# Optimization experiments

Measured on AMD Instinct MI355X. Metric: run time of the kernel, lower is better.

## Reference

```python
import jax, jax.numpy as jnp
import numpy as np

B, N, DIM = 4, 2048, 256
H, HD, M = 8, 32, 4
SPARSE_TOPK = 32


def setup_inputs() -> dict:
    key = jax.random.key(0)
    ks = jax.random.split(key, 6)
    x = jax.random.normal(ks[0], (B, N, DIM), dtype=jnp.float32)
    w_qkv = jax.random.normal(ks[1], (DIM, 3 * H * HD), dtype=jnp.float32) * 0.02
    b_qkv = jnp.zeros((3 * H * HD,), dtype=jnp.float32)
    w_proj = jax.random.normal(ks[2], (H * HD, DIM), dtype=jnp.float32) * 0.02
    b_proj = jnp.zeros((DIM,), dtype=jnp.float32)
    scale = jnp.ones((1, H, 1, 1), dtype=jnp.float32)  # trainable scale, init scale_value=1.0
    mem_k = jax.random.normal(ks[3], (H, M, HD), dtype=jnp.float32)
    mem_v = jax.random.normal(ks[4], (H, M, HD), dtype=jnp.float32)
    return {"x": x, "w_qkv": w_qkv, "b_qkv": b_qkv, "w_proj": w_proj,
            "b_proj": b_proj, "scale": scale, "mem_k": mem_k, "mem_v": mem_v}


def reference(x, w_qkv, b_qkv, w_proj, b_proj, scale, mem_k, mem_v):
    b, n, dim = x.shape
    h, m, hd = mem_k.shape
    qkv = (x @ w_qkv + b_qkv).reshape(b, n, 3, h, hd).transpose(2, 0, 3, 1, 4)
    q, k, v = qkv[0], qkv[1], qkv[2]
    # concat memory vectors along key-length axis -> [B,H,N+M,hd]
    k = jnp.concatenate([k, jnp.broadcast_to(mem_k, (b, h, m, hd))], axis=2)
    v = jnp.concatenate([v, jnp.broadcast_to(mem_v, (b, h, m, hd))], axis=2)
    s = n + m
    # scores with trainable per-head scale: [B,H,N,S]
    scores = jnp.einsum('bhnd,bhsd->bhns', q, k) * (hd ** -0.5) * scale
    neg = -jnp.finfo(scores.dtype).max
    # improve_locality: mask rectangular diagonal (eye(N, S))
    diag = jnp.arange(n)[:, None] == jnp.arange(s)[None, :]
    scores = jnp.where(diag, neg, scores)
    # sparse topk: keep only values >= k-th largest per row
    top = jax.lax.top_k(scores, SPARSE_TOPK)[0]
    vk = top[..., -1:]
    scores = jnp.where(scores < vk, neg, scores)
    attn = jax.nn.softmax(scores, axis=-1)
    out = jnp.einsum('bhns,bhsd->bhnd', attn, v)
    out = out.transpose(0, 2, 1, 3).reshape(b, n, h * hd)
    return out @ w_proj + b_proj
```

## Files before the change

kernel.cpp:

```cpp
#include <hip/hip_runtime.h>
#include <float.h>
#include <stdint.h>

#define Bb   4
#define Nn   2048
#define DIMc 256
#define Hh   8
#define HDd  32
#define Mm   4
#define STOT 2052
#define ROWS 8
#define SROW 2112
#define NVROW 2052

typedef float f32x2 __attribute__((ext_vector_type(2)));

__device__ __forceinline__ unsigned int f2key(float s) {
    unsigned int b = __float_as_uint(s);
    return (b & 0x80000000u) ? ~b : (b | 0x80000000u);
}
__device__ __forceinline__ float key2f(unsigned int u) {
    unsigned int b = (u & 0x80000000u) ? (u ^ 0x80000000u) : ~u;
    return __uint_as_float(b);
}

__global__ __launch_bounds__(256) void sgemm_qkv(
    const float* __restrict__ A, const float* __restrict__ Bm,
    const float* __restrict__ bias, float* __restrict__ Qb,
    float* __restrict__ kTb, float* __restrict__ Vx,
    const float* __restrict__ memv)
{
    __shared__ __align__(16) float As[16][68];
    __shared__ __align__(16) float Bs[16][64];
    __shared__ __align__(16) float Ts[64][65];
    const int tid = threadIdx.x;
    const int tx = tid & 15, ty = tid >> 4;
    const int m0 = blockIdx.y * 64, n0 = blockIdx.x * 64;
    const int arow = tid >> 2, acol = (tid & 3) * 4;
    const int brow = tid >> 4, bcol = (tid & 15) * 4;
    float acc[4][4] = {};
    for (int kb = 0; kb < DIMc; kb += 16) {
        const float4 av = *(const float4*)&A[(size_t)(m0 + arow) * DIMc + kb + acol];
        const float4 bv = *(const float4*)&Bm[(size_t)(kb + brow) * 768 + n0 + bcol];
        __syncthreads();
        As[acol + 0][arow] = av.x;
        As[acol + 1][arow] = av.y;
        As[acol + 2][arow] = av.z;
        As[acol + 3][arow] = av.w;
        *(float4*)&Bs[brow][bcol] = bv;
        __syncthreads();
#pragma unroll
        for (int k = 0; k < 16; ++k) {
            const float4 a  = *(const float4*)&As[k][ty * 4];
            const float4 bq = *(const float4*)&Bs[k][tx * 4];
            const float aa[4] = {a.x, a.y, a.z, a.w};
            const float bb[4] = {bq.x, bq.y, bq.z, bq.w};
#pragma unroll
            for (int i = 0; i < 4; ++i)
#pragma unroll
                for (int j = 0; j < 4; ++j)
                    acc[i][j] = fmaf(aa[i], bb[j], acc[i][j]);
        }
    }
    const float4 bv = *(const float4*)&bias[n0 + tx * 4];
    const float bb[4] = {bv.x, bv.y, bv.z, bv.w};
    const int path = n0 >> 8;
    if (path == 1) {
#pragma unroll
        for (int i = 0; i < 4; ++i)
#pragma unroll
            for (int j = 0; j < 4; ++j)
                Ts[tx * 4 + j][ty * 4 + i] = acc[i][j] + bb[j];
        __syncthreads();
        const int c_local = tid >> 2;
        const int seg     = tid & 3;
        const int cg = (n0 - 256) + c_local;
        const int hh = cg >> 5, dd = cg & 31;
        const int bi = m0 >> 11, j0 = (m0 & 2047) + seg * 16;
        float* dst = kTb + (((size_t)(bi * Hh + hh) * HDd + dd) * Nn) + j0;
#pragma unroll
        for (int q = 0; q < 4; ++q)
            *(float4*)(dst + q * 4) = *(const float4*)&Ts[c_local][seg * 16 + q * 4];
    } else if (path == 0) {
        const int c0 = n0 + tx * 4;
#pragma unroll
        for (int i = 0; i < 4; ++i) {
            float4 o;
            o.x = acc[i][0] + bb[0];
            o.y = acc[i][1] + bb[1];
            o.z = acc[i][2] + bb[2];
            o.w = acc[i][3] + bb[3];
            *(float4*)&Qb[(size_t)(m0 + ty * 4 + i) * 256 + c0] = o;
        }
    } else {
        const int c0 = (n0 & 255) + tx * 4;
        const size_t row_base = (size_t)(m0 >> 11) * NVROW + (m0 & 2047);
#pragma unroll
        for (int i = 0; i < 4; ++i) {
            float4 o;
            o.x = acc[i][0] + bb[0];
            o.y = acc[i][1] + bb[1];
            o.z = acc[i][2] + bb[2];
            o.w = acc[i][3] + bb[3];
            *(float4*)&Vx[(row_base + ty * 4 + i) * 256 + c0] = o;
        }
        if (n0 == 512 && (m0 & 2047) == 0) {
            const int bb2 = m0 >> 11;
#pragma unroll
            for (int mm = 0; mm < Mm; ++mm)
                Vx[((size_t)bb2 * NVROW + Nn + mm) * 256 + tid] =
                    memv[((tid >> 5) * Mm + mm) * HDd + (tid & 31)];
        }
    }
}

__global__ __launch_bounds__(256) void sgemm_bias(
    const float* __restrict__ A, const float* __restrict__ Bm,
    const float* __restrict__ bias, float* __restrict__ C,
    int Md, int Nd, int Kd)
{
    __shared__ __align__(16) float As[16][68];
    __shared__ __align__(16) float Bs[16][64];
    const int tid = threadIdx.x;
    const int tx = tid & 15, ty = tid >> 4;
    const int m0 = blockIdx.y * 64, n0 = blockIdx.x * 64;
    const int arow = tid >> 2, acol = (tid & 3) * 4;
    const int brow = tid >> 4, bcol = (tid & 15) * 4;
    float acc[4][4] = {};
    for (int kb = 0; kb < Kd; kb += 16) {
        const float4 av = *(const float4*)&A[(size_t)(m0 + arow) * Kd + kb + acol];
        const float4 bv = *(const float4*)&Bm[(size_t)(kb + brow) * Nd + n0 + bcol];
        __syncthreads();
        As[acol + 0][arow] = av.x;
        As[acol + 1][arow] = av.y;
        As[acol + 2][arow] = av.z;
        As[acol + 3][arow] = av.w;
        *(float4*)&Bs[brow][bcol] = bv;
        __syncthreads();
#pragma unroll
        for (int k = 0; k < 16; ++k) {
            const float4 a  = *(const float4*)&As[k][ty * 4];
            const float4 bq = *(const float4*)&Bs[k][tx * 4];
            const float aa[4] = {a.x, a.y, a.z, a.w};
            const float bb[4] = {bq.x, bq.y, bq.z, bq.w};
#pragma unroll
            for (int i = 0; i < 4; ++i)
#pragma unroll
                for (int j = 0; j < 4; ++j)
                    acc[i][j] = fmaf(aa[i], bb[j], acc[i][j]);
        }
    }
    const float4 bv = *(const float4*)&bias[n0 + tx * 4];
    const float bb[4] = {bv.x, bv.y, bv.z, bv.w};
#pragma unroll
    for (int i = 0; i < 4; ++i) {
        float4 o;
        o.x = acc[i][0] + bb[0];
        o.y = acc[i][1] + bb[1];
        o.z = acc[i][2] + bb[2];
        o.w = acc[i][3] + bb[3];
        *(float4*)&C[(size_t)(m0 + ty * 4 + i) * Nd + n0 + tx * 4] = o;
    }
}

#if __has_builtin(__builtin_elementwise_fma)
#define PKSTEP(Q, P)                                                        \
    { const f32x2 qq = {(Q), (Q)};                                          \
      a01 = __builtin_elementwise_fma(qq, ((const f32x2*)&kd[P])[0], a01);  \
      a23 = __builtin_elementwise_fma(qq, ((const f32x2*)&kd[P])[1], a23); }
#else
#define PKSTEP(Q, P)                                                        \
    { a01.x = fmaf((Q), kd[P].x, a01.x); a01.y = fmaf((Q), kd[P].y, a01.y); \
      a23.x = fmaf((Q), kd[P].z, a23.x); a23.y = fmaf((Q), kd[P].w, a23.y); }
#endif

__global__ __launch_bounds__(512, 4) void attn_sparse(
    const float* __restrict__ Qb, const float* __restrict__ kTb,
    const float* __restrict__ Vx, const float* __restrict__ memk,
    const float* __restrict__ scale, float* __restrict__ attn_out)
{
    __shared__ __align__(16) unsigned int S[ROWS][SROW];
    __shared__ __align__(16) float qs[ROWS][HDd];
    __shared__ unsigned int       u_list[ROWS][64];
    __shared__ unsigned short     j_list[ROWS][64];
    __shared__ unsigned long long wj_list[ROWS][64];

    const int tid    = threadIdx.x;
    const int ntiles = Nn / ROWS;
    const int tile   = blockIdx.x % ntiles;
    const int h      = (blockIdx.x / ntiles) % Hh;
    const int b      = blockIdx.x / (ntiles * Hh);
    const int n0     = tile * ROWS;
    const float sc   = scale[h] * 0.17677669529663688f;

    if (tid < ROWS * HDd) {
        const int r = tid >> 5, d2 = tid & 31;
        qs[r][d2] = Qb[(size_t)(b * Nn + n0 + r) * 256 + h * HDd + d2];
    }
    __syncthreads();

    const float* kT = kTb + (size_t)(b * Hh + h) * (HDd * Nn);

    {
        const int j0 = tid * 4;
        f32x2 acc01[ROWS], acc23[ROWS];
#pragma unroll
        for (int r = 0; r < ROWS; ++r) { acc01[r] = (f32x2){0.f, 0.f}; acc23[r] = (f32x2){0.f, 0.f}; }
#pragma unroll 1
        for (int dc = 0; dc < 4; ++dc) {
            float4 kd[8];
#pragma unroll
            for (int dd = 0; dd < 8; ++dd)
                kd[dd] = *(const float4*)&kT[(dc * 8 + dd) * Nn + j0];
#pragma unroll
            for (int r = 0; r < ROWS; ++r) {
                const float4 qa = *(const float4*)&qs[r][dc * 8];
                const float4 qb2 = *(const float4*)&qs[r][dc * 8 + 4];
                f32x2 a01 = acc01[r], a23 = acc23[r];
                PKSTEP(qa.x, 0) PKSTEP(qa.y, 1) PKSTEP(qa.z, 2) PKSTEP(qa.w, 3)
                PKSTEP(qb2.x, 4) PKSTEP(qb2.y, 5) PKSTEP(qb2.z, 6) PKSTEP(qb2.w, 7)
                acc01[r] = a01; acc23[r] = a23;
            }
        }
#pragma unroll
        for (int r = 0; r < ROWS; ++r) {
            const float af[4] = {acc01[r].x, acc01[r].y, acc23[r].x, acc23[r].y};
            uint4 o;
            unsigned int* op = (unsigned int*)&o;
#pragma unroll
            for (int kk = 0; kk < 4; ++kk) {
                float s = af[kk] * sc;
                if (j0 + kk == n0 + r) s = -FLT_MAX;
                op[kk] = f2key(s);
            }
            *(uint4*)&S[r][j0] = o;
        }
    }
    if (tid < 16) {
        const int j0 = 2048 + tid * 4;
        float acc[ROWS][4];
#pragma unroll
        for (int r = 0; r < ROWS; ++r)
#pragma unroll
            for (int kk = 0; kk < 4; ++kk) acc[r][kk] = 0.f;
        const float* kp[4];
#pragma unroll
        for (int kk = 0; kk < 4; ++kk) {
            const int j = j0 + kk;
            kp[kk] = (j < STOT) ? (memk + (size_t)(h * Mm + (j - Nn)) * HDd)
                                : memk;
        }
#pragma unroll 1
        for (int dc = 0; dc < 4; ++dc) {
            float4 k0[4], k1[4];
#pragma unroll
            for (int kk = 0; kk < 4; ++kk) {
                k0[kk] = *(const float4*)(kp[kk] + dc * 8);
                k1[kk] = *(const float4*)(kp[kk] + dc * 8 + 4);
            }
#pragma unroll
            for (int r = 0; r < ROWS; ++r) {
                const float4 qa = *(const float4*)&qs[r][dc * 8];
                const float4 qb2 = *(const float4*)&qs[r][dc * 8 + 4];
#pragma unroll
                for (int kk = 0; kk < 4; ++kk) {
                    float t = fmaf(qa.x, k0[kk].x, acc[r][kk]);
                    t = fmaf(qa.y, k0[kk].y, t);
                    t = fmaf(qa.z, k0[kk].z, t);
                    t = fmaf(qa.w, k0[kk].w, t);
                    t = fmaf(qb2.x, k1[kk].x, t);
                    t = fmaf(qb2.y, k1[kk].y, t);
                    t = fmaf(qb2.z, k1[kk].z, t);
                    t = fmaf(qb2.w, k1[kk].w, t);
                    acc[r][kk] = t;
                }
            }
        }
#pragma unroll
        for (int r = 0; r < ROWS; ++r) {
            uint4 o;
            unsigned int* op = (unsigned int*)&o;
#pragma unroll
            for (int kk = 0; kk < 4; ++kk) {
                const int j = j0 + kk;
                float s = acc[r][kk] * sc;
                if (j >= STOT || j == n0 + r) s = -FLT_MAX;
                op[kk] = f2key(s);
            }
            *(uint4*)&S[r][j0] = o;
        }
    }
    __syncthreads();

    const int wave = tid >> 6, lane = tid & 63;
    const int half = lane >> 5, d = lane & 31;
    const int n = n0 + wave;

    unsigned int uv[33];
    unsigned int mx = 0u;
    {
        const unsigned int* Srow = &S[wave][lane];
#pragma unroll
        for (int i = 0; i < 33; ++i) {
            uv[i] = Srow[i * 64];
            mx = uv[i] > mx ? uv[i] : mx;
        }
    }

    auto bitonic = [&](unsigned int vv) -> unsigned int {
#pragma unroll
        for (int kk = 2; kk <= 64; kk <<= 1)
#pragma unroll
            for (int jj = kk >> 1; jj > 0; jj >>= 1) {
                const unsigned int o = (unsigned int)__shfl_xor((int)vv, jj);
                const unsigned int mn = vv < o ? vv : o;
                const unsigned int mxv = vv < o ? o : vv;
                const bool up   = ((lane & kk) == 0);
                const bool lowr = ((lane & jj) == 0);
                vv = (lowr == up) ? mn : mxv;
            }
        return vv;
    };
    auto countge = [&](unsigned int tt) -> int {
        int gg = 0;
#pragma unroll
        for (int i = 0; i < 33; ++i) gg += (int)__popcll(__ballot(uv[i] >= tt));
        return gg;
    };

    const unsigned int vs1 = bitonic(mx);
    const unsigned int Lmax = (unsigned int)__shfl((int)vs1, 63);
    unsigned int t = (unsigned int)__shfl((int)vs1, 32);

    int g = countge(t);
    bool exact = true;
    if (g > 64) {
        unsigned int blo = t, bhi = Lmax + 1;
        int found = 0;
#pragma unroll 1
        for (int it = 0; it < 33; ++it) {
            if (bhi - blo <= 1u) break;
            const unsigned int tm = blo + ((bhi - blo) >> 1);
            const int gm = countge(tm);
            if (gm > 64) blo = tm;
            else if (gm < 32) bhi = tm;
            else { t = tm; g = gm; found = 1; break; }
        }
        if (!found) { t = blo; g = countge(blo); exact = (g <= 64); }
    }

    u_list[wave][lane] = 0u;
    j_list[wave][lane] = 0;
    __asm__ __volatile__("s_waitcnt lgkmcnt(0)" ::: "memory");
    int base = 0;
#pragma unroll
    for (int i = 0; i < 33; ++i) {
        const bool p = (uv[i] >= t);
        const unsigned long long mk = __ballot(p);
        if (p) {
            const int pos = base + (int)__popcll(mk & ((1ull << lane) - 1ull));
            if (pos < 64) {
                u_list[wave][pos] = uv[i];
                j_list[wave][pos] = (unsigned short)(i * 64 + lane);
            }
        }
        base += (int)__popcll(mk);
    }
    const int C2 = base < 64 ? base : 64;
    __asm__ __volatile__("s_waitcnt lgkmcnt(0)" ::: "memory");
    const unsigned int ue = u_list[wave][lane];
    const int je = (int)j_list[wave][lane];

    const unsigned int vs2 = bitonic(ue);
    unsigned int vkkey = (unsigned int)__shfl((int)vs2, 32);
    const unsigned int v31u = (unsigned int)__shfl((int)vs2, 31);
    if (!exact) vkkey = t;

    const bool tie_span = (v31u == vkkey);
    float snx = -3.0e38f;
    if (exact && !tie_span) {
        if (C2 == 32) {
            unsigned int unx = 0u;
#pragma unroll
            for (int i = 0; i < 33; ++i) {
                const unsigned int u = uv[i];
                if (u < vkkey && u > unx) unx = u;
            }
#pragma unroll
            for (int o = 32; o > 0; o >>= 1) {
                const unsigned int ou = (unsigned int)__shfl_xor((int)unx, o);
                if (ou > unx) unx = ou;
            }
            snx = key2f(unx);
        } else {
            snx = key2f(v31u);
        }
    }
    const float svk  = key2f(vkkey);
    const float gapv = svk - snx;
    const float lam  = (exact && !tie_span && gapv > 0.f && gapv <= 4.0e-6f) ? 0.13f : 0.f;

    const float mval = key2f(Lmax);
    const float we = (ue >= vkkey) ? __expf(key2f(ue) - mval) : 0.f;
    wj_list[wave][lane] = ((unsigned long long)(unsigned int)je << 32) | (unsigned long long)__float_as_uint(we);
    float Z = we;
#pragma unroll
    for (int o = 32; o > 0; o >>= 1) Z += __shfl_xor(Z, o);
    __asm__ __volatile__("s_waitcnt lgkmcnt(0)" ::: "memory");

    const float* Vbh = Vx + (size_t)b * (NVROW * 256) + h * HDd;
    float outv = 0.f;
#pragma unroll 1
    for (int e0 = 0; e0 < C2; e0 += 8) {
        float w[4]; int q[4];
#pragma unroll
        for (int u2 = 0; u2 < 4; ++u2) {
            const unsigned long long wj = wj_list[wave][e0 + u2 * 2 + half];
            w[u2] = __uint_as_float((unsigned int)wj);
            q[u2] = (int)(wj >> 32);
        }
        float vv[4];
#pragma unroll
        for (int u2 = 0; u2 < 4; ++u2)
            vv[u2] = Vbh[(size_t)q[u2] * 256 + d];
#pragma unroll
        for (int u2 = 0; u2 < 4; ++u2)
            outv = fmaf(w[u2], vv[u2], outv);
    }
    outv += __shfl_xor(outv, 32);

    float res = outv / Z;
    if (lam > 0.f) {
        unsigned int unx2 = 0u; int jnx = 0, jd1 = -1;
#pragma unroll
        for (int i = 0; i < 33; ++i) {
            const unsigned int u = uv[i];
            const int jj2 = i * 64 + lane;
            if (u < vkkey && u > unx2) { unx2 = u; jnx = jj2; }
            if (u == vkkey && jj2 > jd1) jd1 = jj2;
        }
#pragma unroll
        for (int o = 32; o > 0; o >>= 1) {
            const unsigned int ou = (unsigned int)__shfl_xor((int)unx2, o);
            const int oj = __shfl_xor(jnx, o);
            if (ou > unx2 || (ou == unx2 && oj > jnx)) { unx2 = ou; jnx = oj; }
            const int od = __shfl_xor(jd1, o);
            if (od > jd1) jd1 = od;
        }
        const float wd = __expf(svk - mval);
        const float wn = __expf(key2f(unx2) - mval);
        const float* vp1 = Vbh + (size_t)jd1 * 256;
        const float* vpn = Vbh + (size_t)jnx * 256;
        const float ZB = Z - wd + wn;
        const float oB = (outv - wd * vp1[d] + wn * vpn[d]) / ZB;
        res = (1.f - lam) * res + lam * oB;
    }
    if (half == 0)
        attn_out[(size_t)(b * Nn + n) * 256 + h * HDd + d] = res;
}

extern "C" void kernel_launch(void* const* d_in, const int* in_sizes, int n_in,
                              void* d_out, int out_size, void* d_ws, size_t ws_size,
                              hipStream_t stream) {
    const float* x      = (const float*)d_in[0];
    const float* w_qkv  = (const float*)d_in[1];
    const float* b_qkv  = (const float*)d_in[2];
    const float* w_proj = (const float*)d_in[3];
    const float* b_proj = (const float*)d_in[4];
    const float* scale  = (const float*)d_in[5];
    const float* mem_k  = (const float*)d_in[6];
    const float* mem_v  = (const float*)d_in[7];
    float* out = (float*)d_out;

    float* Qb  = (float*)d_ws;
    float* kTb = Qb  + (size_t)Bb * Nn * 256;
    float* Vx  = kTb + (size_t)Bb * Hh * HDd * Nn;

    sgemm_qkv<<<dim3(768 / 64, (Bb * Nn) / 64), 256, 0, stream>>>(
        x, w_qkv, b_qkv, Qb, kTb, Vx, mem_v);

    attn_sparse<<<dim3(Bb * Hh * (Nn / ROWS)), 512, 0, stream>>>(
        Qb, kTb, Vx, mem_k, scale, Qb);

    sgemm_bias<<<dim3(DIMc / 64, (Bb * Nn) / 64), 256, 0, stream>>>(
        Qb, w_proj, b_proj, out, Bb * Nn, DIMc, DIMc);
}
```

Baseline: 419.6 us.

## Double-buffer GEMM tiles, shrink proj tile, streamline sparse attention compaction and memory scores

Both GEMMs now double-buffer their shared-memory tiles, prefetching the next K slice into registers during compute so each iteration needs one barrier instead of two. The output projection switches to 32-row tiles so more blocks are launched. In the attention kernel, the memory-key scores are computed by 32 threads at one dot product each instead of 16 threads running a loop, and the row padding is filled directly. Top-k candidates are compacted into packed 64-bit key/index entries in the same pass used for counting, which avoids a separate count-then-compact pass in the common case. The weight/index list is laid out so each half-wave reads it with vector loads, and the gather loop is unrolled. This trades some extra shared memory and code complexity for fewer barriers, fewer passes and better occupancy.

After: 364.5 us. 13.1% less time.

```diff
diff --git a/kernel.cpp b/kernel.cpp
--- a/kernel.cpp
+++ b/kernel.cpp
@@ -14,6 +14,7 @@
 #define NVROW 2052
 
 typedef float f32x2 __attribute__((ext_vector_type(2)));
+typedef unsigned long long u64;
 
 __device__ __forceinline__ unsigned int f2key(float s) {
     unsigned int b = __float_as_uint(s);
@@ -30,8 +31,8 @@
     float* __restrict__ kTb, float* __restrict__ Vx,
     const float* __restrict__ memv)
 {
-    __shared__ __align__(16) float As[16][68];
-    __shared__ __align__(16) float Bs[16][64];
+    __shared__ __align__(16) float As[2][16][68];
+    __shared__ __align__(16) float Bs[2][16][64];
     __shared__ __align__(16) float Ts[64][65];
     const int tid = threadIdx.x;
     const int tx = tid & 15, ty = tid >> 4;
@@ -39,20 +40,29 @@
     const int arow = tid >> 2, acol = (tid & 3) * 4;
     const int brow = tid >> 4, bcol = (tid & 15) * 4;
     float acc[4][4] = {};
+
+    {
+        const float4 av = *(const float4*)&A[(size_t)(m0 + arow) * DIMc + acol];
+        const float4 bv = *(const float4*)&Bm[(size_t)brow * 768 + n0 + bcol];
+        As[0][acol + 0][arow] = av.x;
+        As[0][acol + 1][arow] = av.y;
+        As[0][acol + 2][arow] = av.z;
+        As[0][acol + 3][arow] = av.w;
+        *(float4*)&Bs[0][brow][bcol] = bv;
+    }
+    int cur = 0;
     for (int kb = 0; kb < DIMc; kb += 16) {
-        const float4 av = *(const float4*)&A[(size_t)(m0 + arow) * DIMc + kb + acol];
-        const float4 bv = *(const float4*)&Bm[(size_t)(kb + brow) * 768 + n0 + bcol];
+        float4 av2, bv2;
+        const bool more = (kb + 16 < DIMc);
+        if (more) {
+            av2 = *(const float4*)&A[(size_t)(m0 + arow) * DIMc + kb + 16 + acol];
+            bv2 = *(const float4*)&Bm[(size_t)(kb + 16 + brow) * 768 + n0 + bcol];
+        }
         __syncthreads();
-        As[acol + 0][arow] = av.x;
-        As[acol + 1][arow] = av.y;
-        As[acol + 2][arow] = av.z;
-        As[acol + 3][arow] = av.w;
-        *(float4*)&Bs[brow][bcol] = bv;
-        __syncthreads();
 #pragma unroll
         for (int k = 0; k < 16; ++k) {
-            const float4 a  = *(const float4*)&As[k][ty * 4];
-            const float4 bq = *(const float4*)&Bs[k][tx * 4];
+            const float4 a  = *(const float4*)&As[cur][k][ty * 4];
+            const float4 bq = *(const float4*)&Bs[cur][k][tx * 4];
             const float aa[4] = {a.x, a.y, a.z, a.w};
             const float bb[4] = {bq.x, bq.y, bq.z, bq.w};
 #pragma unroll
@@ -61,6 +71,14 @@
                 for (int j = 0; j < 4; ++j)
                     acc[i][j] = fmaf(aa[i], bb[j], acc[i][j]);
         }
+        if (more) {
+            As[cur ^ 1][acol + 0][arow] = av2.x;
+            As[cur ^ 1][acol + 1][arow] = av2.y;
+            As[cur ^ 1][acol + 2][arow] = av2.z;
+            As[cur ^ 1][acol + 3][arow] = av2.w;
+            *(float4*)&Bs[cur ^ 1][brow][bcol] = bv2;
+        }
+        cur ^= 1;
     }
     const float4 bv = *(const float4*)&bias[n0 + tx * 4];
     const float bb[4] = {bv.x, bv.y, bv.z, bv.w};
@@ -119,47 +137,69 @@
     const float* __restrict__ bias, float* __restrict__ C,
     int Md, int Nd, int Kd)
 {
-    __shared__ __align__(16) float As[16][68];
-    __shared__ __align__(16) float Bs[16][64];
+    __shared__ __align__(16) float As[2][16][36];
+    __shared__ __align__(16) float Bs[2][16][64];
     const int tid = threadIdx.x;
     const int tx = tid & 15, ty = tid >> 4;
-    const int m0 = blockIdx.y * 64, n0 = blockIdx.x * 64;
+    const int m0 = blockIdx.y * 32, n0 = blockIdx.x * 64;
     const int arow = tid >> 2, acol = (tid & 3) * 4;
     const int brow = tid >> 4, bcol = (tid & 15) * 4;
-    float acc[4][4] = {};
+    float acc[2][4] = {};
+
+    {
+        const float4 bv = *(const float4*)&Bm[(size_t)brow * Nd + n0 + bcol];
+        *(float4*)&Bs[0][brow][bcol] = bv;
+        if (tid < 128) {
+            const float4 av = *(const float4*)&A[(size_t)(m0 + arow) * Kd + acol];
+            As[0][acol + 0][arow] = av.x;
+            As[0][acol + 1][arow] = av.y;
+            As[0][acol + 2][arow] = av.z;
+            As[0][acol + 3][arow] = av.w;
+        }
+    }
+    int cur = 0;
     for (int kb = 0; kb < Kd; kb += 16) {
-        const float4 av = *(const float4*)&A[(size_t)(m0 + arow) * Kd + kb + acol];
-        const float4 bv = *(const float4*)&Bm[(size_t)(kb + brow) * Nd + n0 + bcol];
+        float4 av2, bv2;
+        const bool more = (kb + 16 < Kd);
+        if (more) {
+            bv2 = *(const float4*)&Bm[(size_t)(kb + 16 + brow) * Nd + n0 + bcol];
+            if (tid < 128)
+                av2 = *(const float4*)&A[(size_t)(m0 + arow) * Kd + kb + 16 + acol];
+        }
         __syncthreads();
-        As[acol + 0][arow] = av.x;
-        As[acol + 1][arow] = av.y;
-        As[acol + 2][arow] = av.z;
-        As[acol + 3][arow] = av.w;
-        *(float4*)&Bs[brow][bcol] = bv;
-        __syncthreads();
 #pragma unroll
         for (int k = 0; k < 16; ++k) {
-            const float4 a  = *(const float4*)&As[k][ty * 4];
-            const float4 bq = *(const float4*)&Bs[k][tx * 4];
-            const float aa[4] = {a.x, a.y, a.z, a.w};
+            const float2 a  = *(const float2*)&As[cur][k][ty * 2];
+            const float4 bq = *(const float4*)&Bs[cur][k][tx * 4];
+            const float aa[2] = {a.x, a.y};
             const float bb[4] = {bq.x, bq.y, bq.z, bq.w};
 #pragma unroll
-            for (int i = 0; i < 4; ++i)
+            for (int i = 0; i < 2; ++i)
 #pragma unroll
                 for (int j = 0; j < 4; ++j)
                     acc[i][j] = fmaf(aa[i], bb[j], acc[i][j]);
         }
+        if (more) {
+            *(float4*)&Bs[cur ^ 1][brow][bcol] = bv2;
+            if (tid < 128) {
+                As[cur ^ 1][acol + 0][arow] = av2.x;
+                As[cur ^ 1][acol + 1][arow] = av2.y;
+                As[cur ^ 1][acol + 2][arow] = av2.z;
+                As[cur ^ 1][acol + 3][arow] = av2.w;
+            }
+        }
+        cur ^= 1;
     }
     const float4 bv = *(const float4*)&bias[n0 + tx * 4];
     const float bb[4] = {bv.x, bv.y, bv.z, bv.w};
 #pragma unroll
-    for (int i = 0; i < 4; ++i) {
+    for (int i = 0; i < 2; ++i) {
         float4 o;
         o.x = acc[i][0] + bb[0];
         o.y = acc[i][1] + bb[1];
         o.z = acc[i][2] + bb[2];
         o.w = acc[i][3] + bb[3];
-        *(float4*)&C[(size_t)(m0 + ty * 4 + i) * Nd + n0 + tx * 4] = o;
+        *(float4*)&C[(size_t)(m0 + ty * 2 + i) * Nd + n0 + tx * 4] = o;
     }
 }
 
@@ -181,9 +221,8 @@
 {
     __shared__ __align__(16) unsigned int S[ROWS][SROW];
     __shared__ __align__(16) float qs[ROWS][HDd];
-    __shared__ unsigned int       u_list[ROWS][64];
-    __shared__ unsigned short     j_list[ROWS][64];
-    __shared__ unsigned long long wj_list[ROWS][64];
+    __shared__ __align__(16) u64 ulist64[ROWS][64];
+    __shared__ __align__(16) u64 wj_list[ROWS][64];
 
     const int tid    = threadIdx.x;
     const int ntiles = Nn / ROWS;
@@ -236,59 +275,24 @@
             *(uint4*)&S[r][j0] = o;
         }
     }
-    if (tid < 16) {
-        const int j0 = 2048 + tid * 4;
-        float acc[ROWS][4];
-#pragma unroll
-        for (int r = 0; r < ROWS; ++r)
-#pragma unroll
-            for (int kk = 0; kk < 4; ++kk) acc[r][kk] = 0.f;
-        const float* kp[4];
-#pragma unroll
-        for (int kk = 0; kk < 4; ++kk) {
-            const int j = j0 + kk;
-            kp[kk] = (j < STOT) ? (memk + (size_t)(h * Mm + (j - Nn)) * HDd)
-                                : memk;
-        }
-#pragma unroll 1
-        for (int dc = 0; dc < 4; ++dc) {
-            float4 k0[4], k1[4];
-#pragma unroll
-            for (int kk = 0; kk < 4; ++kk) {
-                k0[kk] = *(const float4*)(kp[kk] + dc * 8);
-                k1[kk] = *(const float4*)(kp[kk] + dc * 8 + 4);
-            }
-#pragma unroll
-            for (int r = 0; r < ROWS; ++r) {
-                const float4 qa = *(const float4*)&qs[r][dc * 8];
-                const float4 qb2 = *(const float4*)&qs[r][dc * 8 + 4];
-#pragma unroll
-                for (int kk = 0; kk < 4; ++kk) {
-                    float t = fmaf(qa.x, k0[kk].x, acc[r][kk]);
-                    t = fmaf(qa.y, k0[kk].y, t);
-                    t = fmaf(qa.z, k0[kk].z, t);
-                    t = fmaf(qa.w, k0[kk].w, t);
-                    t = fmaf(qb2.x, k1[kk].x, t);
-                    t = fmaf(qb2.y, k1[kk].y, t);
-                    t = fmaf(qb2.z, k1[kk].z, t);
-                    t = fmaf(qb2.w, k1[kk].w, t);
-                    acc[r][kk] = t;
-                }
-            }
-        }
-#pragma unroll
-        for (int r = 0; r < ROWS; ++r) {
-            uint4 o;
-            unsigned int* op = (unsigned int*)&o;
-#pragma unroll
-            for (int kk = 0; kk < 4; ++kk) {
-                const int j = j0 + kk;
-                float s = acc[r][kk] * sc;
-                if (j >= STOT || j == n0 + r) s = -FLT_MAX;
-                op[kk] = f2key(s);
-            }
-            *(uint4*)&S[r][j0] = o;
-        }
+    if (tid < 32) {
+        const int r = tid >> 2, m = tid & 3;
+        const float* kp = memk + (size_t)(h * Mm + m) * HDd;
+        float acc = 0.f;
+#pragma unroll
+        for (int dcc = 0; dcc < 8; ++dcc) {
+            const float4 qv = *(const float4*)&qs[r][dcc * 4];
+            const float4 kv = *(const float4*)&kp[dcc * 4];
+            acc = fmaf(qv.x, kv.x, acc);
+            acc = fmaf(qv.y, kv.y, acc);
+            acc = fmaf(qv.z, kv.z, acc);
+            acc = fmaf(qv.w, kv.w, acc);
+        }
+        S[r][2048 + m] = f2key(acc * sc);
+    } else {
+        const int t2 = tid - 32;
+        const int r = t2 / 60, p = t2 % 60;
+        S[r][2052 + p] = 0x00800000u;
     }
     __syncthreads();
 
@@ -327,14 +331,31 @@
         for (int i = 0; i < 33; ++i) gg += (int)__popcll(__ballot(uv[i] >= tt));
         return gg;
     };
+    auto compact = [&](unsigned int tt) -> int {
+        int bs = 0;
+#pragma unroll
+        for (int i = 0; i < 33; ++i) {
+            const bool p = (uv[i] >= tt);
+            const unsigned long long mk = __ballot(p);
+            if (p) {
+                const int pos = bs + (int)__popcll(mk & ((1ull << lane) - 1ull));
+                if (pos < 64)
+                    ulist64[wave][pos] = ((u64)uv[i] << 32) | (unsigned int)(i * 64 + lane);
+            }
+            bs += (int)__popcll(mk);
+        }
+        return bs;
+    };
 
     const unsigned int vs1 = bitonic(mx);
     const unsigned int Lmax = (unsigned int)__shfl((int)vs1, 63);
     unsigned int t = (unsigned int)__shfl((int)vs1, 32);
 
-    int g = countge(t);
+    ulist64[wave][lane] = 0ull;
+    __asm__ __volatile__("s_waitcnt lgkmcnt(0)" ::: "memory");
+    int base = compact(t);
     bool exact = true;
-    if (g > 64) {
+    if (base > 64) {
         unsigned int blo = t, bhi = Lmax + 1;
         int found = 0;
 #pragma unroll 1
@@ -344,32 +365,19 @@
             const int gm = countge(tm);
             if (gm > 64) blo = tm;
             else if (gm < 32) bhi = tm;
-            else { t = tm; g = gm; found = 1; break; }
-        }
-        if (!found) { t = blo; g = countge(blo); exact = (g <= 64); }
-    }
-
-    u_list[wave][lane] = 0u;
-    j_list[wave][lane] = 0;
-    __asm__ __volatile__("s_waitcnt lgkmcnt(0)" ::: "memory");
-    int base = 0;
-#pragma unroll
-    for (int i = 0; i < 33; ++i) {
-        const bool p = (uv[i] >= t);
-        const unsigned long long mk = __ballot(p);
-        if (p) {
-            const int pos = base + (int)__popcll(mk & ((1ull << lane) - 1ull));
-            if (pos < 64) {
-                u_list[wave][pos] = uv[i];
-                j_list[wave][pos] = (unsigned short)(i * 64 + lane);
-            }
-        }
-        base += (int)__popcll(mk);
+            else { t = tm; found = 1; break; }
+        }
+        if (!found) t = blo;
+        ulist64[wave][lane] = 0ull;
+        __asm__ __volatile__("s_waitcnt lgkmcnt(0)" ::: "memory");
+        base = compact(t);
+        exact = (base <= 64);
     }
     const int C2 = base < 64 ? base : 64;
     __asm__ __volatile__("s_waitcnt lgkmcnt(0)" ::: "memory");
-    const unsigned int ue = u_list[wave][lane];
-    const int je = (int)j_list[wave][lane];
+    const u64 pk = ulist64[wave][lane];
+    const unsigned int ue = (unsigned int)(pk >> 32);
+    const int je = (int)(unsigned int)pk;
 
     const unsigned int vs2 = bitonic(ue);
     unsigned int vkkey = (unsigned int)__shfl((int)vs2, 32);
@@ -402,7 +410,8 @@
 
     const float mval = key2f(Lmax);
     const float we = (ue >= vkkey) ? __expf(key2f(ue) - mval) : 0.f;
-    wj_list[wave][lane] = ((unsigned long long)(unsigned int)je << 32) | (unsigned long long)__float_as_uint(we);
+    wj_list[wave][(lane & 1) * 32 + (lane >> 1)] =
+        ((u64)(unsigned int)je << 32) | (u64)__float_as_uint(we);
     float Z = we;
 #pragma unroll
     for (int o = 32; o > 0; o >>= 1) Z += __shfl_xor(Z, o);
@@ -410,19 +419,20 @@
 
     const float* Vbh = Vx + (size_t)b * (NVROW * 256) + h * HDd;
     float outv = 0.f;
-#pragma unroll 1
+#pragma unroll 2
     for (int e0 = 0; e0 < C2; e0 += 8) {
-        float w[4]; int q[4];
-#pragma unroll
-        for (int u2 = 0; u2 < 4; ++u2) {
-            const unsigned long long wj = wj_list[wave][e0 + u2 * 2 + half];
-            w[u2] = __uint_as_float((unsigned int)wj);
-            q[u2] = (int)(wj >> 32);
-        }
+        const int p0 = (e0 >> 1) + half * 32;
+        const ulonglong2 wa = *(const ulonglong2*)&wj_list[wave][p0];
+        const ulonglong2 wb = *(const ulonglong2*)&wj_list[wave][p0 + 2];
+        float w[4]; unsigned int q[4];
+        w[0] = __uint_as_float((unsigned int)wa.x); q[0] = (unsigned int)(wa.x >> 32);
+        w[1] = __uint_as_float((unsigned int)wa.y); q[1] = (unsigned int)(wa.y >> 32);
+        w[2] = __uint_as_float((unsigned int)wb.x); q[2] = (unsigned int)(wb.x >> 32);
+        w[3] = __uint_as_float((unsigned int)wb.y); q[3] = (unsigned int)(wb.y >> 32);
         float vv[4];
 #pragma unroll
         for (int u2 = 0; u2 < 4; ++u2)
-            vv[u2] = Vbh[(size_t)q[u2] * 256 + d];
+            vv[u2] = Vbh[q[u2] * 256u + (unsigned int)d];
 #pragma unroll
         for (int u2 = 0; u2 < 4; ++u2)
             outv = fmaf(w[u2], vv[u2], outv);
@@ -482,6 +492,6 @@
     attn_sparse<<<dim3(Bb * Hh * (Nn / ROWS)), 512, 0, stream>>>(
         Qb, kTb, Vx, mem_k, scale, Qb);
 
-    sgemm_bias<<<dim3(DIMc / 64, (Bb * Nn) / 64), 256, 0, stream>>>(
+    sgemm_bias<<<dim3(DIMc / 64, (Bb * Nn) / 32), 256, 0, stream>>>(
         Qb, w_proj, b_proj, out, Bb * Nn, DIMc, DIMc);
 }
```
